# Kernel optimization log

Measured on AMD Instinct MI355X. Metric: run time of the kernel, lower is better.

Reference implementation:

```python
import jax, jax.numpy as jnp
import numpy as np

V, D, NH, L, T, B = 32000, 768, 12, 4, 2048, 1
HD = D // NH
THETA = 10000.0
EPS = 1e-5


def setup_inputs() -> dict:
    key = jax.random.key(0)
    ks = jax.random.split(key, 12)
    s = 0.02
    return {
        "idx": jax.random.randint(ks[0], (B, T), 0, V),
        "wte": jax.random.normal(ks[1], (V, D), jnp.float32) * s,
        "ln1_w": jnp.ones((L, D), jnp.float32),
        "attn_w": jax.random.normal(ks[2], (L, 3 * D, D), jnp.float32) * s,
        "attnproj_w": jax.random.normal(ks[3], (L, D, D), jnp.float32) * s,
        "ln2_w": jnp.ones((L, D), jnp.float32),
        "fc_w": jax.random.normal(ks[4], (L, 4 * D, D), jnp.float32) * s,
        "fc_b": jnp.zeros((L, 4 * D), jnp.float32),
        "proj_w": jax.random.normal(ks[5], (L, D, 4 * D), jnp.float32) * s,
        "proj_b": jnp.zeros((L, D), jnp.float32),
        "lnf_w": jnp.ones((D,), jnp.float32),
        "unemb_b": jnp.zeros((V,), jnp.float32),
    }


def _ln(x, w):
    mu = jnp.mean(x, axis=-1, keepdims=True)
    var = jnp.mean(jnp.square(x - mu), axis=-1, keepdims=True)
    return (x - mu) * jax.lax.rsqrt(var + EPS) * w


def _rope(x, cos, sin):
    # x: [B,NH,T,HD]; cos/sin: [T,HD//2]
    x1, x2 = x[..., : HD // 2], x[..., HD // 2 :]
    return jnp.concatenate([x1 * cos - x2 * sin, x1 * sin + x2 * cos], axis=-1)


def _forward(idx, wte, ln1_w, attn_w, attnproj_w, ln2_w, fc_w, fc_b, proj_w, proj_b, lnf_w, unemb_b):
    x = wte[idx]  # [B,T,D]
    inv_freq = 1.0 / (THETA ** (jnp.arange(0, HD, 2, dtype=jnp.float32) / HD))  # [HD/2]
    t = jnp.arange(T, dtype=jnp.float32)
    freqs = jnp.outer(t, inv_freq)  # [T, HD/2]
    cos, sin = jnp.cos(freqs), jnp.sin(freqs)
    causal = jnp.tril(jnp.ones((T, T), bool))
    scale = 1.0 / jnp.sqrt(jnp.asarray(HD, x.dtype))
    for l in range(L):
        h = _ln(x, ln1_w[l])
        qkv = h @ attn_w[l].T  # [B,T,3D]
        q, k, v = jnp.split(qkv, 3, axis=-1)
        q = q.reshape(B, T, NH, HD).transpose(0, 2, 1, 3)
        k = k.reshape(B, T, NH, HD).transpose(0, 2, 1, 3)
        v = v.reshape(B, T, NH, HD).transpose(0, 2, 1, 3)
        q, k = _rope(q, cos, sin), _rope(k, cos, sin)
        att = jnp.einsum("bhqd,bhkd->bhqk", q, k) * scale
        att = jnp.where(causal, att, -jnp.inf)
        att = jax.nn.softmax(att, axis=-1)
        y = jnp.einsum("bhqk,bhkd->bhqd", att, v)
        y = y.transpose(0, 2, 1, 3).reshape(B, T, D)
        x = x + y @ attnproj_w[l].T
        h = _ln(x, ln2_w[l])
        m = jax.nn.gelu(h @ fc_w[l].T + fc_b[l], approximate=False)
        x = x + m @ proj_w[l].T + proj_b[l]
    x = _ln(x, lnf_w)
    return x @ wte.T + unemb_b  # tied unembedding, [B,T,V]


def reference(idx, wte, ln1_w, attn_w, attnproj_w, ln2_w, fc_w, fc_b, proj_w, proj_b, lnf_w, unemb_b):
    return _forward(idx, wte, ln1_w, attn_w, attnproj_w, ln2_w, fc_w, fc_b, proj_w, proj_b, lnf_w, unemb_b)
```

## Files before the change

### kernel.cpp

```cpp
#include <hip/hip_runtime.h>
#include <hip/hip_bf16.h>

typedef __bf16 bf16_t;
typedef __bf16 bf16x8 __attribute__((ext_vector_type(8)));
typedef __bf16 bf16x4 __attribute__((ext_vector_type(4)));
typedef float  f32x4  __attribute__((ext_vector_type(4)));

__device__ __forceinline__ void gl_lds16(const void* g, void* l) {
    __builtin_amdgcn_global_load_lds(
        (__attribute__((address_space(1))) void*)g,
        (__attribute__((address_space(3))) void*)l, 16, 0, 0);
}

template <int N>
__device__ __forceinline__ void wait_vm() {
    if constexpr (N == 0)      asm volatile("s_waitcnt vmcnt(0)" ::: "memory");
    else if constexpr (N == 3) asm volatile("s_waitcnt vmcnt(3)" ::: "memory");
    else                       asm volatile("s_waitcnt vmcnt(4)" ::: "memory");
}

__global__ void cvt_kernel(const float* __restrict__ in, bf16_t* __restrict__ out,
                           int n4) {
    const int i = blockIdx.x * 256 + threadIdx.x;
    if (i < n4) {
        const float4 v = ((const float4*)in)[i];
        bf16x4 o;
        o.x = (bf16_t)v.x; o.y = (bf16_t)v.y; o.z = (bf16_t)v.z; o.w = (bf16_t)v.w;
        ((bf16x4*)out)[i] = o;
    }
}

__global__ void cvt4_kernel(const float* __restrict__ s0, const float* __restrict__ s1,
                            const float* __restrict__ s2, const float* __restrict__ s3,
                            bf16_t* __restrict__ d0, bf16_t* __restrict__ d1,
                            bf16_t* __restrict__ d2, bf16_t* __restrict__ d3,
                            int n0, int n1, int n2, int n3) {
    int j = blockIdx.x * 256 + threadIdx.x;
    const float* s; bf16_t* d;
    if (j < n0) { s = s0; d = d0; }
    else {
        j -= n0;
        if (j < n1) { s = s1; d = d1; }
        else {
            j -= n1;
            if (j < n2) { s = s2; d = d2; }
            else {
                j -= n2;
                if (j >= n3) return;
                s = s3; d = d3;
            }
        }
    }
    const float4 v = ((const float4*)s)[j];
    bf16x4 o;
    o.x = (bf16_t)v.x; o.y = (bf16_t)v.y; o.z = (bf16_t)v.z; o.w = (bf16_t)v.w;
    ((bf16x4*)d)[j] = o;
}

__global__ void rope_table(float* __restrict__ tab) {
    const int i = blockIdx.x * 256 + threadIdx.x;
    const int t = i >> 5, f = i & 31;
    const float inv_freq = __powf(10000.0f, -(float)f * (1.0f / 32.0f));
    const float ang = (float)t * inv_freq;
    float s, c;
    __sincosf(ang, &s, &c);
    tab[2 * i]     = c;
    tab[2 * i + 1] = s;
}

__global__ void embed_kernel(const int* __restrict__ idx,
                             const float* __restrict__ wte,
                             float* __restrict__ x) {
    const int t = blockIdx.x;
    const int row = idx[t];
    const float4* w = (const float4*)(wte + (size_t)row * 768);
    float4* o = (float4*)(x + (size_t)t * 768);
    if (threadIdx.x < 192) o[threadIdx.x] = w[threadIdx.x];
}

__global__ __launch_bounds__(256) void ln_kernel(const float* __restrict__ x,
                                                 const float* __restrict__ w,
                                                 bf16_t* __restrict__ out) {
    const int t = blockIdx.x, tid = threadIdx.x;
    __shared__ float red[256];
    const float* xr = x + (size_t)t * 768;
    const float v0 = xr[tid], v1 = xr[tid + 256], v2 = xr[tid + 512];
    red[tid] = v0 + v1 + v2;
    __syncthreads();
    for (int s = 128; s > 0; s >>= 1) {
        if (tid < s) red[tid] += red[tid + s];
        __syncthreads();
    }
    const float mu = red[0] * (1.0f / 768.0f);
    __syncthreads();
    const float d0 = v0 - mu, d1 = v1 - mu, d2 = v2 - mu;
    red[tid] = d0 * d0 + d1 * d1 + d2 * d2;
    __syncthreads();
    for (int s = 128; s > 0; s >>= 1) {
        if (tid < s) red[tid] += red[tid + s];
        __syncthreads();
    }
    const float rstd = rsqrtf(red[0] * (1.0f / 768.0f) + 1e-5f);
    bf16_t* orow = out + (size_t)t * 768;
    orow[tid]       = (bf16_t)(d0 * rstd * w[tid]);
    orow[tid + 256] = (bf16_t)(d1 * rstd * w[tid + 256]);
    orow[tid + 512] = (bf16_t)(d2 * rstd * w[tid + 512]);
}

__global__ __launch_bounds__(256) void attn_mfma(const bf16_t* __restrict__ Qb,
                                                 const bf16_t* __restrict__ Kb,
                                                 const bf16_t* __restrict__ Vt,
                                                 bf16_t* __restrict__ y) {
    const int qt = (int)gridDim.x - 1 - (int)blockIdx.x;
    const int h  = blockIdx.y;
    const int q0 = qt * 64;
    const int tid = threadIdx.x;
    const int w = tid >> 6, lane = tid & 63;
    const int lg = lane >> 4;
    const int ll = lane & 15;

    __shared__ bf16_t Ks[64 * 64];
    __shared__ bf16_t Vs[64 * 64];
    __shared__ bf16_t Ps[64 * 64];

    bf16x8 aq0, aq1;
    {
        const bf16_t* qp = Qb + ((size_t)h * 2048 + q0 + w * 16 + ll) * 64 + lg * 8;
        aq0 = *(const bf16x8*)qp;
        aq1 = *(const bf16x8*)(qp + 32);
    }

    f32x4 o[4];
    #pragma unroll
    for (int i = 0; i < 4; ++i) o[i] = (f32x4)(0.0f);
    float m_i[4], l_i[4];
    #pragma unroll
    for (int r = 0; r < 4; ++r) { m_i[r] = -3e38f; l_i[r] = 0.0f; }

    const int srow0 = tid >> 3;
    const int srow1 = srow0 + 32;
    const int sc16  = tid & 7;

    const bf16_t* Kbase = Kb + (size_t)h * 2048 * 64;
    const bf16_t* Vbase = Vt + (size_t)h * 64 * 2048;

    bf16x8 pk0, pk1, pv0, pv1;
    {
        const bf16_t* kg = Kbase;
        pk0 = *(const bf16x8*)(kg + srow0 * 64 + sc16 * 8);
        pk1 = *(const bf16x8*)(kg + srow1 * 64 + sc16 * 8);
        pv0 = *(const bf16x8*)(Vbase + (size_t)srow0 * 2048 + sc16 * 8);
        pv1 = *(const bf16x8*)(Vbase + (size_t)srow1 * 2048 + sc16 * 8);
    }

    for (int kt = 0; kt <= qt; ++kt) {
        __syncthreads();
        *(bf16x8*)((char*)(Ks + srow0 * 64) + ((sc16 * 16) ^ ((srow0 & 7) << 4))) = pk0;
        *(bf16x8*)((char*)(Ks + srow1 * 64) + ((sc16 * 16) ^ ((srow1 & 7) << 4))) = pk1;
        *(bf16x8*)((char*)(Vs + srow0 * 64) + ((sc16 * 16) ^ ((srow0 & 7) << 4))) = pv0;
        *(bf16x8*)((char*)(Vs + srow1 * 64) + ((sc16 * 16) ^ ((srow1 & 7) << 4))) = pv1;
        __syncthreads();

        if (kt < qt) {
            const bf16_t* kg = Kbase + (size_t)((kt + 1) * 64) * 64;
            pk0 = *(const bf16x8*)(kg + srow0 * 64 + sc16 * 8);
            pk1 = *(const bf16x8*)(kg + srow1 * 64 + sc16 * 8);
            const bf16_t* vg = Vbase + (kt + 1) * 64;
            pv0 = *(const bf16x8*)(vg + (size_t)srow0 * 2048 + sc16 * 8);
            pv1 = *(const bf16x8*)(vg + (size_t)srow1 * 2048 + sc16 * 8);
        }

        f32x4 sacc[4];
        #pragma unroll
        for (int kb = 0; kb < 4; ++kb) {
            const int krow = kb * 16 + ll;
            const char* kr = (const char*)(Ks + krow * 64);
            const int sw = (krow & 7) << 4;
            const bf16x8 b0 = *(const bf16x8*)(kr + ((lg * 16) ^ sw));
            const bf16x8 b1 = *(const bf16x8*)(kr + ((64 + lg * 16) ^ sw));
            sacc[kb] = __builtin_amdgcn_mfma_f32_16x16x32_bf16(aq0, b0, (f32x4)(0.0f), 0, 0, 0);
            sacc[kb] = __builtin_amdgcn_mfma_f32_16x16x32_bf16(aq1, b1, sacc[kb], 0, 0, 0);
        }

        float sc_[4][4];
        const bool diag = (kt == qt);
        #pragma unroll
        for (int kb = 0; kb < 4; ++kb) {
            #pragma unroll
            for (int r = 0; r < 4; ++r) {
                float v = sacc[kb][r];
                if (diag && (kb * 16 + ll) > (w * 16 + lg * 4 + r)) v = -3e38f;
                sc_[kb][r] = v;
            }
        }
        float rmax[4];
        #pragma unroll
        for (int r = 0; r < 4; ++r)
            rmax[r] = fmaxf(fmaxf(sc_[0][r], sc_[1][r]), fmaxf(sc_[2][r], sc_[3][r]));
        #pragma unroll
        for (int st = 0; st < 4; ++st) {
            const int off = 1 << st;
            #pragma unroll
            for (int r = 0; r < 4; ++r)
                rmax[r] = fmaxf(rmax[r], __shfl_xor(rmax[r], off));
        }
        float alpha[4], rsum[4];
        #pragma unroll
        for (int r = 0; r < 4; ++r) {
            const float mn = fmaxf(m_i[r], rmax[r]);
            alpha[r] = __expf(m_i[r] - mn);
            m_i[r] = mn;
            rsum[r] = 0.0f;
        }
        #pragma unroll
        for (int kb = 0; kb < 4; ++kb) {
            #pragma unroll
            for (int r = 0; r < 4; ++r) {
                const float p = __expf(sc_[kb][r] - m_i[r]);
                sc_[kb][r] = p;
                rsum[r] += p;
            }
        }
        #pragma unroll
        for (int st = 0; st < 4; ++st) {
            const int off = 1 << st;
            #pragma unroll
            for (int r = 0; r < 4; ++r)
                rsum[r] += __shfl_xor(rsum[r], off);
        }
        #pragma unroll
        for (int r = 0; r < 4; ++r) l_i[r] = l_i[r] * alpha[r] + rsum[r];

        #pragma unroll
        for (int r = 0; r < 4; ++r) {
            const int prow = w * 16 + lg * 4 + r;
            char* pb = (char*)(Ps + prow * 64);
            const int sw = (prow & 7) << 4;
            #pragma unroll
            for (int kb = 0; kb < 4; ++kb)
                *(bf16_t*)(pb + (((kb * 16 + ll) * 2) ^ sw)) = (bf16_t)sc_[kb][r];
        }

        #pragma unroll
        for (int db = 0; db < 4; ++db)
            #pragma unroll
            for (int r = 0; r < 4; ++r) o[db][r] *= alpha[r];

        #pragma unroll
        for (int ks = 0; ks < 2; ++ks) {
            const int arow = w * 16 + ll;
            const bf16x8 ap = *(const bf16x8*)((const char*)(Ps + arow * 64) +
                                ((ks * 64 + lg * 16) ^ ((arow & 7) << 4)));
            #pragma unroll
            for (int db = 0; db < 4; ++db) {
                const int vrow = db * 16 + ll;
                const bf16x8 bv = *(const bf16x8*)((const char*)(Vs + vrow * 64) +
                                    ((ks * 64 + lg * 16) ^ ((vrow & 7) << 4)));
                o[db] = __builtin_amdgcn_mfma_f32_16x16x32_bf16(ap, bv, o[db], 0, 0, 0);
            }
        }
    }

    #pragma unroll
    for (int r = 0; r < 4; ++r) {
        const float inv = 1.0f / l_i[r];
        bf16_t* yo = y + (size_t)(q0 + w * 16 + lg * 4 + r) * 768 + h * 64 + ll;
        #pragma unroll
        for (int db = 0; db < 4; ++db)
            yo[db * 16] = (bf16_t)(o[db][r] * inv);
    }
}

template <int FLAGS, int BM, int BN>
__global__ __launch_bounds__((BN == 256) ? 512 : 256)
void gemm_bt(const bf16_t* __restrict__ A,
             const bf16_t* __restrict__ B,
             const float* __restrict__ bias,
             float* __restrict__ C32,
             bf16_t* __restrict__ Cb,
             const float* __restrict__ rt,
             bf16_t* __restrict__ Qd,
             bf16_t* __restrict__ Kd,
             bf16_t* __restrict__ Vd,
             int M, int N, int K) {
    constexpr bool HAS_BIAS = (FLAGS & 1) != 0;
    constexpr bool HAS_RES  = (FLAGS & 2) != 0;
    constexpr bool HAS_GELU = (FLAGS & 4) != 0;
    constexpr bool OUT_BF16 = (FLAGS & 8) != 0;
    constexpr bool UNEMB    = (FLAGS & 16) != 0;
    constexpr bool QKV      = (FLAGS & 32) != 0;
    constexpr bool WIDE     = (BN == 256);
    constexpr int  WM       = WIDE ? 64 : ((BM == 128) ? 64 : 32);
    constexpr int  MI       = WM / 16;
    constexpr int  NLOADS   = WIDE ? 3 : ((BM == 128) ? 4 : 3);

    __shared__ bf16_t smem[2 * (BM + BN) * 32];
    bf16_t* As0 = smem;
    bf16_t* Bs0 = As0 + BM * 32;
    bf16_t* As1 = Bs0 + BN * 32;
    bf16_t* Bs1 = As1 + BM * 32;

    const int tid = threadIdx.x;
    const int w = tid >> 6, lane = tid & 63;

    int bm, bn;
    if constexpr (UNEMB) {
        const int bid  = (int)blockIdx.y * (int)gridDim.x + (int)blockIdx.x;
        const int per  = ((int)gridDim.x * (int)gridDim.y) >> 3;
        const int nid  = (bid & 7) * per + (bid >> 3);
        bm = (nid & 15) * BM;
        bn = (nid >> 4) * BN;
    } else {
        bm = blockIdx.y * BM;
        bn = blockIdx.x * BN;
    }
    int wm, wn;
    if constexpr (WIDE) { wm = (w >> 2) * 64; wn = (w & 3) * 64; }
    else                { wm = (w >> 1) * WM; wn = (w & 1) * 64; }

    const int sc = (lane & 3) * 8;
    const int srB = w * 32 + (lane >> 2);
    const bf16_t* gB0 = B + (size_t)(bn + srB) * K + sc;
    const bf16_t* gB1 = gB0 + (size_t)16 * K;
    const int ldsB = (w * 32) * 32;
    const int srA = (!WIDE && BM == 128) ? srB : (w * 16 + (lane >> 2));
    const bf16_t* gA0 = A + (size_t)(bm + srA) * K + sc;
    const bf16_t* gA1 = gA0 + (size_t)16 * K;
    const int ldsA = ((!WIDE && BM == 128) ? (w * 32) : (w * 16)) * 32;

    const int mrow  = lane & 15;
    const int khalf = (lane >> 4) * 8;

    f32x4 acc[MI][4];
    #pragma unroll
    for (int i = 0; i < MI; ++i)
        #pragma unroll
        for (int j = 0; j < 4; ++j) acc[i][j] = (f32x4)(0.0f);

    auto stage = [&](bf16_t* Ap, bf16_t* Bp, int kk) {
        gl_lds16(gA0 + kk, Ap + ldsA);
        if constexpr (!WIDE && BM == 128) gl_lds16(gA1 + kk, Ap + ldsA + 16 * 32);
        gl_lds16(gB0 + kk, Bp + ldsB);
        gl_lds16(gB1 + kk, Bp + ldsB + 16 * 32);
    };
    auto compute = [&](const bf16_t* Ap, const bf16_t* Bp) {
        bf16x8 af[MI], bfr[4];
        #pragma unroll
        for (int i = 0; i < MI; ++i)
            af[i] = *(const bf16x8*)(Ap + (wm + i * 16 + mrow) * 32 + khalf);
        #pragma unroll
        for (int j = 0; j < 4; ++j)
            bfr[j] = *(const bf16x8*)(Bp + (wn + j * 16 + mrow) * 32 + khalf);
        #pragma unroll
        for (int i = 0; i < MI; ++i)
            #pragma unroll
            for (int j = 0; j < 4; ++j)
                acc[i][j] = __builtin_amdgcn_mfma_f32_16x16x32_bf16(
                    af[i], bfr[j], acc[i][j], 0, 0, 0);
    };

    stage(As0, Bs0, 0);
    for (int k0 = 0; k0 < K; k0 += 64) {
        stage(As1, Bs1, k0 + 32);
        wait_vm<NLOADS>();
        __builtin_amdgcn_s_barrier();
        __builtin_amdgcn_sched_barrier(0);
        compute(As0, Bs0);
        __builtin_amdgcn_sched_barrier(0);
        __builtin_amdgcn_s_barrier();
        const bool more = (k0 + 64) < K;
        if (more) stage(As0, Bs0, k0 + 64);
        if (more) wait_vm<NLOADS>(); else wait_vm<0>();
        __builtin_amdgcn_s_barrier();
        __builtin_amdgcn_sched_barrier(0);
        compute(As1, Bs1);
        __builtin_amdgcn_sched_barrier(0);
        __builtin_amdgcn_s_barrier();
    }

    const int ccol = lane & 15;
    const int crow = (lane >> 4) * 4;

    if constexpr (QKV) {
        const int col0  = bn + wn;
        const int which = col0 / 768;
        const int hh    = (col0 % 768) >> 6;
        #pragma unroll
        for (int i = 0; i < MI; ++i) {
            const int row0 = bm + wm + i * 16 + crow;
            if (which == 2) {
                #pragma unroll
                for (int j = 0; j < 4; ++j) {
                    const int d = j * 16 + ccol;
                    bf16x4 v4;
                    #pragma unroll
                    for (int r = 0; r < 4; ++r) v4[r] = (bf16_t)acc[i][j][r];
                    *(bf16x4*)(Vd + (size_t)(hh * 64 + d) * 2048 + row0) = v4;
                }
            } else {
                bf16_t* dst0 = (which ? Kd : Qd) + (size_t)hh * 2048 * 64;
                const float scq = which ? 1.0f : 0.125f;
                #pragma unroll
                for (int j = 0; j < 2; ++j) {
                    const int d = j * 16 + ccol;
                    #pragma unroll
                    for (int r = 0; r < 4; ++r) {
                        const int t = row0 + r;
                        const float2 cs = ((const float2*)rt)[t * 32 + d];
                        const float x1 = acc[i][j][r], x2 = acc[i][j + 2][r];
                        bf16_t* dp = dst0 + (size_t)t * 64 + d;
                        dp[0]  = (bf16_t)((x1 * cs.x - x2 * cs.y) * scq);
                        dp[32] = (bf16_t)((x1 * cs.y + x2 * cs.x) * scq);
                    }
                }
            }
        }
        return;
    }

    #pragma unroll
    for (int i = 0; i < MI; ++i) {
        #pragma unroll
        for (int j = 0; j < 4; ++j) {
            const int col = bn + wn + j * 16 + ccol;
            #pragma unroll
            for (int r = 0; r < 4; ++r) {
                const int row = bm + wm + i * 16 + crow + r;
                float v = acc[i][j][r];
                if constexpr (HAS_BIAS) v += bias[col];
                if constexpr (HAS_GELU) v = 0.5f * v * (1.0f + erff(v * 0.70710678f));
                const size_t off = (size_t)row * N + col;
                if constexpr (HAS_RES) v += C32[off];
                if constexpr (OUT_BF16) Cb[off] = (bf16_t)v;
                else C32[off] = v;
            }
        }
    }
}

extern "C" void kernel_launch(void* const* d_in, const int* in_sizes, int n_in,
                              void* d_out, int out_size, void* d_ws, size_t ws_size,
                              hipStream_t stream) {
    const int T = 2048, D = 768, NH = 12, L = 4, V = 32000;
    const int D3 = 3 * D, D4 = 4 * D;

    const int*   idx        = (const int*)d_in[0];
    const float* wte        = (const float*)d_in[1];
    const float* ln1_w      = (const float*)d_in[2];
    const float* attn_w     = (const float*)d_in[3];
    const float* attnproj_w = (const float*)d_in[4];
    const float* ln2_w      = (const float*)d_in[5];
    const float* fc_w       = (const float*)d_in[6];
    const float* fc_b       = (const float*)d_in[7];
    const float* proj_w     = (const float*)d_in[8];
    const float* proj_b     = (const float*)d_in[9];
    const float* lnf_w      = (const float*)d_in[10];
    const float* unemb_b    = (const float*)d_in[11];
    float* out = (float*)d_out;

    char* p = (char*)d_ws;
    float*  X      = (float*)p;   p += (size_t)T * D * 4;
    bf16_t* Hb     = (bf16_t*)p;  p += (size_t)T * D * 2;
    bf16_t* Mb     = (bf16_t*)p;  p += (size_t)T * D4 * 2;
    bf16_t* wte_b  = (bf16_t*)p;  p += (size_t)V * D * 2;
    bf16_t* w_attn = (bf16_t*)p;  p += (size_t)L * D3 * D * 2;
    bf16_t* w_apr  = (bf16_t*)p;  p += (size_t)L * D * D * 2;
    bf16_t* w_fc   = (bf16_t*)p;  p += (size_t)L * D4 * D * 2;
    bf16_t* w_proj = (bf16_t*)p;  p += (size_t)L * D * D4 * 2;
    float*  rtab   = (float*)p;   p += (size_t)T * 32 * 2 * 4;

    bf16_t* Qb  = wte_b;
    bf16_t* Kbf = Qb  + (size_t)NH * T * 64;
    bf16_t* Vtg = Kbf + (size_t)NH * T * 64;

    embed_kernel<<<T, 256, 0, stream>>>(idx, wte, X);
    rope_table<<<T * 32 / 256, 256, 0, stream>>>(rtab);

    const int na = L * D3 * D / 4, nb = L * D * D / 4;
    const int nc = L * D4 * D / 4, nd = L * D * D4 / 4;
    const int ntot = na + nb + nc + nd;
    cvt4_kernel<<<(ntot + 255) / 256, 256, 0, stream>>>(
        attn_w, attnproj_w, fc_w, proj_w,
        w_attn, w_apr, w_fc, w_proj, na, nb, nc, nd);

    for (int l = 0; l < L; ++l) {
        ln_kernel<<<T, 256, 0, stream>>>(X, ln1_w + (size_t)l * D, Hb);
        gemm_bt<32, 128, 128><<<dim3(D3 / 128, T / 128), 256, 0, stream>>>(
            Hb, w_attn + (size_t)l * D3 * D, nullptr, nullptr, nullptr,
            rtab, Qb, Kbf, Vtg, T, D3, D);
        attn_mfma<<<dim3(T / 64, NH), 256, 0, stream>>>(Qb, Kbf, Vtg, Hb);
        gemm_bt<2, 64, 128><<<dim3(D / 128, T / 64), 256, 0, stream>>>(
            Hb, w_apr + (size_t)l * D * D, nullptr, X, nullptr,
            nullptr, nullptr, nullptr, nullptr, T, D, D);
        ln_kernel<<<T, 256, 0, stream>>>(X, ln2_w + (size_t)l * D, Hb);
        gemm_bt<13, 128, 128><<<dim3(D4 / 128, T / 128), 256, 0, stream>>>(
            Hb, w_fc + (size_t)l * D4 * D, fc_b + (size_t)l * D4, nullptr, Mb,
            nullptr, nullptr, nullptr, nullptr, T, D4, D);
        gemm_bt<3, 64, 128><<<dim3(D / 128, T / 64), 256, 0, stream>>>(
            Mb, w_proj + (size_t)l * D * D4, proj_b + (size_t)l * D, X, nullptr,
            nullptr, nullptr, nullptr, nullptr, T, D, D4);
    }

    ln_kernel<<<T, 256, 0, stream>>>(X, lnf_w, Hb);
    {
        const int n4 = V * D / 4;
        cvt_kernel<<<(n4 + 255) / 256, 256, 0, stream>>>(wte, wte_b, n4);
    }
    gemm_bt<17, 128, 256><<<dim3(T / 128, V / 256), 512, 0, stream>>>(
        Hb, wte_b, unemb_b, out, nullptr,
        nullptr, nullptr, nullptr, nullptr, T, V, D);
}
```

Measured before the change: 1.214 ms.

## Fuse small kernels, double-buffer attention K/V tiles, add lazy softmax rescale

Result: slower. 1.252 ms (+3.2%).

```diff
diff --git a/kernel.cpp b/kernel.cpp
--- a/kernel.cpp
+++ b/kernel.cpp
@@ -57,54 +57,79 @@
     ((bf16x4*)d)[j] = o;
 }
 
-__global__ void rope_table(float* __restrict__ tab) {
-    const int i = blockIdx.x * 256 + threadIdx.x;
-    const int t = i >> 5, f = i & 31;
-    const float inv_freq = __powf(10000.0f, -(float)f * (1.0f / 32.0f));
-    const float ang = (float)t * inv_freq;
-    float s, c;
-    __sincosf(ang, &s, &c);
-    tab[2 * i]     = c;
-    tab[2 * i + 1] = s;
-}
-
 __global__ void embed_kernel(const int* __restrict__ idx,
                              const float* __restrict__ wte,
-                             float* __restrict__ x) {
+                             float* __restrict__ x,
+                             float* __restrict__ tab) {
     const int t = blockIdx.x;
-    const int row = idx[t];
-    const float4* w = (const float4*)(wte + (size_t)row * 768);
-    float4* o = (float4*)(x + (size_t)t * 768);
-    if (threadIdx.x < 192) o[threadIdx.x] = w[threadIdx.x];
+    if (threadIdx.x < 192) {
+        const int row = idx[t];
+        const float4* w = (const float4*)(wte + (size_t)row * 768);
+        float4* o = (float4*)(x + (size_t)t * 768);
+        o[threadIdx.x] = w[threadIdx.x];
+    } else if (threadIdx.x < 224) {
+        const int i = threadIdx.x - 192;
+        const float inv_freq = __powf(10000.0f, -(float)i * (1.0f / 32.0f));
+        const float ang = (float)t * inv_freq;
+        float s, c;
+        __sincosf(ang, &s, &c);
+        tab[2 * (t * 32 + i)]     = c;
+        tab[2 * (t * 32 + i) + 1] = s;
+    }
+}
+
+__device__ __forceinline__ void ln_row(const float* __restrict__ xr,
+                                       const float* __restrict__ w,
+                                       bf16_t* __restrict__ orow,
+                                       int tid, float* a1, float* a2) {
+    const int wv = tid >> 6, lane = tid & 63;
+    const float v0 = xr[tid], v1 = xr[tid + 256], v2 = xr[tid + 512];
+    float s1 = v0 + v1 + v2;
+    float s2 = v0 * v0 + v1 * v1 + v2 * v2;
+    #pragma unroll
+    for (int off = 32; off >= 1; off >>= 1) {
+        s1 += __shfl_xor(s1, off);
+        s2 += __shfl_xor(s2, off);
+    }
+    if (lane == 0) { a1[wv] = s1; a2[wv] = s2; }
+    __syncthreads();
+    const float t1 = a1[0] + a1[1] + a1[2] + a1[3];
+    const float t2 = a2[0] + a2[1] + a2[2] + a2[3];
+    const float mu = t1 * (1.0f / 768.0f);
+    const float var = t2 * (1.0f / 768.0f) - mu * mu;
+    const float rstd = rsqrtf(var + 1e-5f);
+    orow[tid]       = (bf16_t)((v0 - mu) * rstd * w[tid]);
+    orow[tid + 256] = (bf16_t)((v1 - mu) * rstd * w[tid + 256]);
+    orow[tid + 512] = (bf16_t)((v2 - mu) * rstd * w[tid + 512]);
 }
 
 __global__ __launch_bounds__(256) void ln_kernel(const float* __restrict__ x,
                                                  const float* __restrict__ w,
                                                  bf16_t* __restrict__ out) {
-    const int t = blockIdx.x, tid = threadIdx.x;
-    __shared__ float red[256];
-    const float* xr = x + (size_t)t * 768;
-    const float v0 = xr[tid], v1 = xr[tid + 256], v2 = xr[tid + 512];
-    red[tid] = v0 + v1 + v2;
-    __syncthreads();
-    for (int s = 128; s > 0; s >>= 1) {
-        if (tid < s) red[tid] += red[tid + s];
-        __syncthreads();
-    }
-    const float mu = red[0] * (1.0f / 768.0f);
-    __syncthreads();
-    const float d0 = v0 - mu, d1 = v1 - mu, d2 = v2 - mu;
-    red[tid] = d0 * d0 + d1 * d1 + d2 * d2;
-    __syncthreads();
-    for (int s = 128; s > 0; s >>= 1) {
-        if (tid < s) red[tid] += red[tid + s];
-        __syncthreads();
-    }
-    const float rstd = rsqrtf(red[0] * (1.0f / 768.0f) + 1e-5f);
-    bf16_t* orow = out + (size_t)t * 768;
-    orow[tid]       = (bf16_t)(d0 * rstd * w[tid]);
-    orow[tid + 256] = (bf16_t)(d1 * rstd * w[tid + 256]);
-    orow[tid + 512] = (bf16_t)(d2 * rstd * w[tid + 512]);
+    __shared__ float a1[4], a2[4];
+    const int t = blockIdx.x;
+    ln_row(x + (size_t)t * 768, w, out + (size_t)t * 768, threadIdx.x, a1, a2);
+}
+
+__global__ __launch_bounds__(256) void lncvt_kernel(const float* __restrict__ x,
+                                                    const float* __restrict__ w,
+                                                    bf16_t* __restrict__ out,
+                                                    const float* __restrict__ wte,
+                                                    bf16_t* __restrict__ wte_b,
+                                                    int n4) {
+    if ((int)blockIdx.x >= 2048) {
+        const int i = ((int)blockIdx.x - 2048) * 256 + threadIdx.x;
+        if (i < n4) {
+            const float4 v = ((const float4*)wte)[i];
+            bf16x4 o;
+            o.x = (bf16_t)v.x; o.y = (bf16_t)v.y; o.z = (bf16_t)v.z; o.w = (bf16_t)v.w;
+            ((bf16x4*)wte_b)[i] = o;
+        }
+        return;
+    }
+    __shared__ float a1[4], a2[4];
+    const int t = blockIdx.x;
+    ln_row(x + (size_t)t * 768, w, out + (size_t)t * 768, threadIdx.x, a1, a2);
 }
 
 __global__ __launch_bounds__(256) void attn_mfma(const bf16_t* __restrict__ Qb,
@@ -119,8 +144,8 @@
     const int lg = lane >> 4;
     const int ll = lane & 15;
 
-    __shared__ bf16_t Ks[64 * 64];
-    __shared__ bf16_t Vs[64 * 64];
+    __shared__ bf16_t Ks[2][64 * 64];
+    __shared__ bf16_t Vs[2][64 * 64];
     __shared__ bf16_t Ps[64 * 64];
 
     bf16x8 aq0, aq1;
@@ -140,27 +165,25 @@
     const int srow0 = tid >> 3;
     const int srow1 = srow0 + 32;
     const int sc16  = tid & 7;
+    const int swz0  = (sc16 * 16) ^ ((srow0 & 7) << 4);
+    const int swz1  = (sc16 * 16) ^ ((srow1 & 7) << 4);
 
     const bf16_t* Kbase = Kb + (size_t)h * 2048 * 64;
     const bf16_t* Vbase = Vt + (size_t)h * 64 * 2048;
 
     bf16x8 pk0, pk1, pv0, pv1;
-    {
-        const bf16_t* kg = Kbase;
-        pk0 = *(const bf16x8*)(kg + srow0 * 64 + sc16 * 8);
-        pk1 = *(const bf16x8*)(kg + srow1 * 64 + sc16 * 8);
-        pv0 = *(const bf16x8*)(Vbase + (size_t)srow0 * 2048 + sc16 * 8);
-        pv1 = *(const bf16x8*)(Vbase + (size_t)srow1 * 2048 + sc16 * 8);
-    }
-
+    pk0 = *(const bf16x8*)(Kbase + srow0 * 64 + sc16 * 8);
+    pk1 = *(const bf16x8*)(Kbase + srow1 * 64 + sc16 * 8);
+    pv0 = *(const bf16x8*)(Vbase + (size_t)srow0 * 2048 + sc16 * 8);
+    pv1 = *(const bf16x8*)(Vbase + (size_t)srow1 * 2048 + sc16 * 8);
+    *(bf16x8*)((char*)(Ks[0] + srow0 * 64) + swz0) = pk0;
+    *(bf16x8*)((char*)(Ks[0] + srow1 * 64) + swz1) = pk1;
+    *(bf16x8*)((char*)(Vs[0] + srow0 * 64) + swz0) = pv0;
+    *(bf16x8*)((char*)(Vs[0] + srow1 * 64) + swz1) = pv1;
+    __syncthreads();
+
+    int cur = 0;
     for (int kt = 0; kt <= qt; ++kt) {
-        __syncthreads();
-        *(bf16x8*)((char*)(Ks + srow0 * 64) + ((sc16 * 16) ^ ((srow0 & 7) << 4))) = pk0;
-        *(bf16x8*)((char*)(Ks + srow1 * 64) + ((sc16 * 16) ^ ((srow1 & 7) << 4))) = pk1;
-        *(bf16x8*)((char*)(Vs + srow0 * 64) + ((sc16 * 16) ^ ((srow0 & 7) << 4))) = pv0;
-        *(bf16x8*)((char*)(Vs + srow1 * 64) + ((sc16 * 16) ^ ((srow1 & 7) << 4))) = pv1;
-        __syncthreads();
-
         if (kt < qt) {
             const bf16_t* kg = Kbase + (size_t)((kt + 1) * 64) * 64;
             pk0 = *(const bf16x8*)(kg + srow0 * 64 + sc16 * 8);
@@ -169,12 +192,14 @@
             pv0 = *(const bf16x8*)(vg + (size_t)srow0 * 2048 + sc16 * 8);
             pv1 = *(const bf16x8*)(vg + (size_t)srow1 * 2048 + sc16 * 8);
         }
+        const bf16_t* Kc = Ks[cur];
+        const bf16_t* Vc = Vs[cur];
 
         f32x4 sacc[4];
         #pragma unroll
         for (int kb = 0; kb < 4; ++kb) {
             const int krow = kb * 16 + ll;
-            const char* kr = (const char*)(Ks + krow * 64);
+            const char* kr = (const char*)(Kc + krow * 64);
             const int sw = (krow & 7) << 4;
             const bf16x8 b0 = *(const bf16x8*)(kr + ((lg * 16) ^ sw));
             const bf16x8 b1 = *(const bf16x8*)(kr + ((64 + lg * 16) ^ sw));
@@ -204,14 +229,23 @@
             for (int r = 0; r < 4; ++r)
                 rmax[r] = fmaxf(rmax[r], __shfl_xor(rmax[r], off));
         }
-        float alpha[4], rsum[4];
-        #pragma unroll
-        for (int r = 0; r < 4; ++r) {
-            const float mn = fmaxf(m_i[r], rmax[r]);
-            alpha[r] = __expf(m_i[r] - mn);
-            m_i[r] = mn;
-            rsum[r] = 0.0f;
-        }
+        float growth = -3e38f;
+        #pragma unroll
+        for (int r = 0; r < 4; ++r) growth = fmaxf(growth, rmax[r] - m_i[r]);
+        if (__any(growth > 8.0f)) {
+            #pragma unroll
+            for (int r = 0; r < 4; ++r) {
+                const float mn = fmaxf(m_i[r], rmax[r]);
+                const float a = __expf(m_i[r] - mn);
+                m_i[r] = mn;
+                l_i[r] *= a;
+                #pragma unroll
+                for (int db = 0; db < 4; ++db) o[db][r] *= a;
+            }
+        }
+        float rsum[4];
+        #pragma unroll
+        for (int r = 0; r < 4; ++r) rsum[r] = 0.0f;
         #pragma unroll
         for (int kb = 0; kb < 4; ++kb) {
             #pragma unroll
@@ -229,7 +263,7 @@
                 rsum[r] += __shfl_xor(rsum[r], off);
         }
         #pragma unroll
-        for (int r = 0; r < 4; ++r) l_i[r] = l_i[r] * alpha[r] + rsum[r];
+        for (int r = 0; r < 4; ++r) l_i[r] += rsum[r];
 
         #pragma unroll
         for (int r = 0; r < 4; ++r) {
@@ -242,11 +276,6 @@
         }
 
         #pragma unroll
-        for (int db = 0; db < 4; ++db)
-            #pragma unroll
-            for (int r = 0; r < 4; ++r) o[db][r] *= alpha[r];
-
-        #pragma unroll
         for (int ks = 0; ks < 2; ++ks) {
             const int arow = w * 16 + ll;
             const bf16x8 ap = *(const bf16x8*)((const char*)(Ps + arow * 64) +
@@ -254,11 +283,20 @@
             #pragma unroll
             for (int db = 0; db < 4; ++db) {
                 const int vrow = db * 16 + ll;
-                const bf16x8 bv = *(const bf16x8*)((const char*)(Vs + vrow * 64) +
+                const bf16x8 bv = *(const bf16x8*)((const char*)(Vc + vrow * 64) +
                                     ((ks * 64 + lg * 16) ^ ((vrow & 7) << 4)));
                 o[db] = __builtin_amdgcn_mfma_f32_16x16x32_bf16(ap, bv, o[db], 0, 0, 0);
             }
         }
+
+        if (kt < qt) {
+            *(bf16x8*)((char*)(Ks[cur ^ 1] + srow0 * 64) + swz0) = pk0;
+            *(bf16x8*)((char*)(Ks[cur ^ 1] + srow1 * 64) + swz1) = pk1;
+            *(bf16x8*)((char*)(Vs[cur ^ 1] + srow0 * 64) + swz0) = pv0;
+            *(bf16x8*)((char*)(Vs[cur ^ 1] + srow1 * 64) + swz1) = pv1;
+        }
+        __syncthreads();
+        cur ^= 1;
     }
 
     #pragma unroll
@@ -473,8 +511,7 @@
     bf16_t* Kbf = Qb  + (size_t)NH * T * 64;
     bf16_t* Vtg = Kbf + (size_t)NH * T * 64;
 
-    embed_kernel<<<T, 256, 0, stream>>>(idx, wte, X);
-    rope_table<<<T * 32 / 256, 256, 0, stream>>>(rtab);
+    embed_kernel<<<T, 256, 0, stream>>>(idx, wte, X, rtab);
 
     const int na = L * D3 * D / 4, nb = L * D * D / 4;
     const int nc = L * D4 * D / 4, nd = L * D * D4 / 4;
@@ -501,10 +538,10 @@
             nullptr, nullptr, nullptr, nullptr, T, D, D4);
     }
 
-    ln_kernel<<<T, 256, 0, stream>>>(X, lnf_w, Hb);
     {
         const int n4 = V * D / 4;
-        cvt_kernel<<<(n4 + 255) / 256, 256, 0, stream>>>(wte, wte_b, n4);
+        lncvt_kernel<<<T + (n4 + 255) / 256, 256, 0, stream>>>(
+            X, lnf_w, Hb, wte, wte_b, n4);
     }
     gemm_bt<17, 128, 256><<<dim3(T / 128, V / 256), 512, 0, stream>>>(
         Hb, wte_b, unemb_b, out, nullptr,
```
